# Optimization experiments

Hardware: AMD Instinct MI355X
Metric: run time of the kernel (lower is better)

Reference implementation:

```python
import jax, jax.numpy as jnp
import numpy as np

T = 1024          # num tokens
H = 2048          # hidden_size
NH = 16           # attention heads
NKV = 4           # kv heads (GQA)
HD = 128          # head_dim
E = 32            # num routed experts
K = 4             # top_k
I = 1024          # moe_intermediate_size
NS = 1            # num_shared_experts
EPS = 1e-6
THETA = 600000.0  # rope base
SCALE = HD ** -0.5


def rmsnorm(x, w):
    return x * jax.lax.rsqrt(jnp.mean(x * x, axis=-1, keepdims=True) + EPS) * w


def rope(x, positions):
    # x: [T, n_heads, HD], neox-style rotation on full head_dim
    half = HD // 2
    inv_freq = 1.0 / (THETA ** (jnp.arange(half, dtype=jnp.float32) / half))
    ang = positions.astype(jnp.float32)[:, None] * inv_freq        # [T, half]
    cos = jnp.cos(ang)[:, None, :]
    sin = jnp.sin(ang)[:, None, :]
    x1, x2 = x[..., :half], x[..., half:]
    return jnp.concatenate([x1 * cos - x2 * sin, x1 * sin + x2 * cos], axis=-1)


def setup_inputs() -> dict:
    key = jax.random.key(0)
    ks = jax.random.split(key, 10)
    s = 0.02
    return {
        "hidden_states": jax.random.normal(ks[0], (T, H), dtype=jnp.float32),
        "positions": jnp.arange(T, dtype=jnp.int32),
        "w_rms1": jnp.ones((H,), jnp.float32),
        "w_rms2": jnp.ones((H,), jnp.float32),
        "w_qkv": jax.random.normal(ks[1], ((NH + 2 * NKV) * HD, H), jnp.float32) * s,
        "w_o": jax.random.normal(ks[2], (H, NH * HD), jnp.float32) * s,
        "w_router": jax.random.normal(ks[3], (E, H), jnp.float32) * s,
        "w1": jax.random.normal(ks[4], (E, H, I), jnp.float32) * s,   # expert gate proj
        "w3": jax.random.normal(ks[5], (E, H, I), jnp.float32) * s,   # expert up proj
        "w2": jax.random.normal(ks[6], (E, I, H), jnp.float32) * s,   # expert down proj
        "ws_gate_up": jax.random.normal(ks[7], (2 * I * NS, H), jnp.float32) * s,
        "ws_down": jax.random.normal(ks[8], (H, I * NS), jnp.float32) * s,
    }


def reference(hidden_states, positions, w_rms1, w_rms2, w_qkv, w_o, w_router,
              w1, w3, w2, ws_gate_up, ws_down):
    x = hidden_states
    # ---- attention block ----
    h = rmsnorm(x, w_rms1)
    qkv = h @ w_qkv.T                                   # [T, (NH+2NKV)*HD]
    q = qkv[:, : NH * HD].reshape(T, NH, HD)
    k = qkv[:, NH * HD : (NH + NKV) * HD].reshape(T, NKV, HD)
    v = qkv[:, (NH + NKV) * HD :].reshape(T, NKV, HD)
    q = rope(q, positions)
    k = rope(k, positions)
    rep = NH // NKV
    k = jnp.repeat(k, rep, axis=1)                      # [T, NH, HD]
    v = jnp.repeat(v, rep, axis=1)
    scores = jnp.einsum("thd,shd->hts", q, k) * SCALE   # [NH, T, T]
    causal = jnp.tril(jnp.ones((T, T), dtype=bool))
    scores = jnp.where(causal, scores, -jnp.inf)
    attn = jax.nn.softmax(scores, axis=-1)
    o = jnp.einsum("hts,shd->thd", attn, v).reshape(T, NH * HD)
    x = x + o @ w_o.T                                   # residual
    # ---- MoE block ----
    h2 = rmsnorm(x, w_rms2)
    # router in fp32 (router_dtype default)
    logits = h2.astype(jnp.float32) @ w_router.T        # [T, E]
    probs = jax.nn.softmax(logits, axis=-1)
    topv, topi = jax.lax.top_k(probs, K)                # [T, K]
    topv = topv / jnp.sum(topv, axis=-1, keepdims=True)  # norm_topk_prob
    combine = jnp.zeros((T, E), jnp.float32).at[jnp.arange(T)[:, None], topi].add(topv)
    combine = combine.astype(h2.dtype)                  # routed_scaling_factor = 1.0
    g = jnp.einsum("th,ehi->tei", h2, w1)               # [T, E, I]
    u = jnp.einsum("th,ehi->tei", h2, w3)
    a = jax.nn.silu(g) * u                              # SiluAndMul
    d = jnp.einsum("tei,eih->teh", a, w2)               # [T, E, H]
    routed = jnp.einsum("teh,te->th", d, combine)
    # shared expert MLP
    gu = h2 @ ws_gate_up.T                              # [T, 2*I*NS]
    gs, us = gu[:, : I * NS], gu[:, I * NS :]
    shared = (jax.nn.silu(gs) * us) @ ws_down.T
    return x + routed + shared
```

## Files before the change

kernel.cpp:

```cpp
#include <hip/hip_runtime.h>
#include <hip/hip_bf16.h>
#include <math.h>
#include <stdint.h>

#define T_ 1024
#define H_ 2048
#define NH_ 16
#define NKV_ 4
#define HD_ 128
#define E_ 32
#define TOPK_ 4
#define I_ 1024
#define QKVN_ 3072
#define EPS_ 1e-6f
#define THETA_ 600000.0f
#define SCALE_ 0.08838834764831845f

typedef unsigned short u16;
typedef u16 u16x4 __attribute__((ext_vector_type(4)));
typedef u16 u16x8 __attribute__((ext_vector_type(8)));
typedef __bf16 bf16x8 __attribute__((ext_vector_type(8)));
typedef float f32x4 __attribute__((ext_vector_type(4)));

__device__ __forceinline__ u16 f2b(float f) {
  unsigned u = __builtin_bit_cast(unsigned, f);
  u += 0x7FFFu + ((u >> 16) & 1u);
  return (u16)(u >> 16);
}
__device__ __forceinline__ float b2f(u16 x) {
  unsigned u = ((unsigned)x) << 16;
  return __builtin_bit_cast(float, u);
}
__device__ __forceinline__ int swz8(int r) { return ((r ^ (r >> 3)) & 7) << 3; }
__device__ __forceinline__ int s2(int i) { return (i ^ (i >> 2)) & 3; }

__device__ __forceinline__ void gload16(const void* g, void* l) {
  __builtin_amdgcn_global_load_lds(
      reinterpret_cast<const __attribute__((address_space(1))) unsigned int*>(
          reinterpret_cast<uintptr_t>(g)),
      reinterpret_cast<__attribute__((address_space(3))) unsigned int*>(
          reinterpret_cast<uintptr_t>(l)),
      16, 0, 0);
}

template<int EPI, bool GATHER>
__global__ __launch_bounds__(512, 8) void moe_gemm_k(
    const u16* __restrict__ A, const float* __restrict__ B, const float* __restrict__ B2,
    float* __restrict__ O1, float* __restrict__ O2,
    int NW, int lda, int ldb, int kchunk,
    const int* __restrict__ eoff, const int* __restrict__ slots,
    const float* __restrict__ slotw, long long sBz)
{
  __shared__ u16 As[2][64 * 32];
  __shared__ u16 Bs[2][128 * 32];

  const int e = blockIdx.y >> 3;
  const int mb = blockIdx.y & 7;
  const int goff = eoff[e];
  const int Mloc = eoff[e + 1] - goff;
  const int m0 = mb * 64;
  if (m0 >= Mloc) return;

  const int xx = blockIdx.x;
  const float* Bp;
  float* Op;
  int n0;
  if constexpr (EPI == 0) {
    int wsel = xx >> 3;
    n0 = (xx & 7) * 128;
    Bp = (wsel ? B2 : B) + (long long)e * sBz;
    Op = wsel ? O2 : O1;
  } else {
    n0 = xx * 128;
    Bp = B + (long long)e * sBz;
    Op = O1;
  }
  const int k0base = blockIdx.z * kchunk;
  const u16* Ae = GATHER ? A : (A + (long long)goff * lda);

  const int tid = threadIdx.x;
  const int lane = tid & 63;
  const int wv = tid >> 6;
  const int wm = wv >> 2, wn = wv & 3;

  const u16* Abase = nullptr;
  if (wv < 4) {
    int r = wv * 16 + (lane >> 2);
    int rr = m0 + r;
    if (rr > Mloc - 1) rr = Mloc - 1;
    long long grow = GATHER ? (long long)slots[goff + rr] : (long long)rr;
    Abase = Ae + grow * (long long)lda + (((lane & 3) ^ s2(r)) << 3);
  }

  const int bn = tid & 127;
  const int bkc = tid >> 7;
  const float* Bbase = Bp + (long long)(bkc << 3) * ldb + n0 + bn;
  const int bws = bn * 32 + ((bkc ^ s2(bn)) << 3);

  float br[8];
  auto loadB = [&](int k0) {
    const float* p = Bbase + (long long)k0 * ldb;
    #pragma unroll
    for (int j = 0; j < 8; ++j) br[j] = p[(long long)j * ldb];
  };
  auto writeB = [&](int bf) {
    u16x8 o;
    #pragma unroll
    for (int j = 0; j < 8; ++j) o[j] = f2b(br[j]);
    *(u16x8*)(&Bs[bf][bws]) = o;
  };
  auto stageA = [&](int bf, int k0) {
    if (wv < 4) gload16(Abase + k0, &As[bf][wv * 512]);
  };

  f32x4 acc[2][2];
  #pragma unroll
  for (int m = 0; m < 2; ++m)
    #pragma unroll
    for (int n = 0; n < 2; ++n)
      acc[m][n] = f32x4{0.f, 0.f, 0.f, 0.f};

  const int kg = lane >> 4;
  const int cr = lane & 15;

  int aoff[2], boff[2];
  #pragma unroll
  for (int m = 0; m < 2; ++m) {
    int r = wm * 32 + m * 16 + cr;
    aoff[m] = r * 32 + ((kg ^ s2(r)) << 3);
  }
  #pragma unroll
  for (int n = 0; n < 2; ++n) {
    int c = wn * 32 + n * 16 + cr;
    boff[n] = c * 32 + ((kg ^ s2(c)) << 3);
  }

  loadB(k0base);
  stageA(0, k0base);
  writeB(0);
  __syncthreads();

  int buf = 0;
  for (int ks = 0; ks < kchunk; ks += 32) {
    bool more = (ks + 32) < kchunk;
    if (more) { loadB(k0base + ks + 32); stageA(buf ^ 1, k0base + ks + 32); }
    const u16* Ap = &As[buf][0];
    const u16* Bq = &Bs[buf][0];
    bf16x8 af[2], bfr[2];
    #pragma unroll
    for (int m = 0; m < 2; ++m)
      af[m] = __builtin_bit_cast(bf16x8, *(const u16x8*)(Ap + aoff[m]));
    #pragma unroll
    for (int n = 0; n < 2; ++n)
      bfr[n] = __builtin_bit_cast(bf16x8, *(const u16x8*)(Bq + boff[n]));
    #pragma unroll
    for (int m = 0; m < 2; ++m)
      #pragma unroll
      for (int n = 0; n < 2; ++n)
        acc[m][n] = __builtin_amdgcn_mfma_f32_16x16x32_bf16(af[m], bfr[n], acc[m][n], 0, 0, 0);
    if (more) writeB(buf ^ 1);
    __syncthreads();
    buf ^= 1;
  }

  const int rq = lane >> 4;
  #pragma unroll
  for (int m = 0; m < 2; ++m) {
    #pragma unroll
    for (int j = 0; j < 4; ++j) {
      int row = m0 + wm * 32 + m * 16 + rq * 4 + j;
      if (row >= Mloc) continue;
      if constexpr (EPI == 0) {
        float* dst = Op + (long long)(goff + row) * NW;
        #pragma unroll
        for (int n = 0; n < 2; ++n) {
          int col = n0 + wn * 32 + n * 16 + cr;
          dst[col] = acc[m][n][j];
        }
      } else {
        int tok = slots[goff + row];
        float wgt = slotw[goff + row];
        float* dst = Op + (long long)tok * NW;
        #pragma unroll
        for (int n = 0; n < 2; ++n) {
          int col = n0 + wn * 32 + n * 16 + cr;
          atomicAdd(dst + col, wgt * acc[m][n][j]);
        }
      }
    }
  }
}

template<typename TB, bool BTL, bool GROUPED, bool GATHER, int EPI>
__global__ __launch_bounds__(256) void gemm_k(
    const u16* __restrict__ A, const TB* __restrict__ B, const TB* __restrict__ B2,
    u16* __restrict__ Cb, u16* __restrict__ Cb2, float* __restrict__ Cf,
    const float* __restrict__ res1, const float* __restrict__ res2,
    int M, int N, int K, int lda, int ldb, int ldc,
    float alpha, int causal, int mbmax, int yhalf,
    const int* __restrict__ eoff, const int* __restrict__ slots,
    const float* __restrict__ slotw,
    long long sAz, long long sBz, long long sCz, int bdivz)
{
  __shared__ u16 As[2][8192];
  __shared__ u16 Bs[2][8192];

  int m0, n0, Mloc, goff = 0;
  const u16* Ae = A;
  const TB* Be = B;
  u16* Cw = Cb;
  if (GROUPED) {
    int e = blockIdx.x / mbmax;
    int mb = blockIdx.x - e * mbmax;
    goff = eoff[e];
    Mloc = eoff[e + 1] - goff;
    m0 = mb * 128;
    if (m0 >= Mloc) return;
    int by = blockIdx.y;
    if (yhalf && by >= yhalf) {
      n0 = (by - yhalf) * 128;
      Be = B2 + (long long)e * sBz;
      Cw = Cb2;
    } else {
      n0 = by * 128;
      Be = B + (long long)e * sBz;
    }
    if (!GATHER) Ae = A + (long long)goff * lda;
  } else {
    m0 = blockIdx.x * 128;
    n0 = blockIdx.y * 128;
    Mloc = M;
    long long z = blockIdx.z;
    Ae = A + z * sAz;
    Be = B + (long long)(z / bdivz) * sBz;
    if (Cb) Cw = Cb + z * sCz;
    if (causal == 1 && n0 > m0 + 127) return;
  }

  const int tid = threadIdx.x;
  const int lane = tid & 63;
  const int wv = tid >> 6;
  const int wr = wv >> 1, wc = wv & 1;

  int kend = K;
  if (causal == 2) { int ke = m0 + 128; if (ke < kend) kend = ke; }

  f32x4 acc[4][4];
  #pragma unroll
  for (int i = 0; i < 4; ++i)
    #pragma unroll
    for (int j = 0; j < 4; ++j)
      acc[i][j] = f32x4{0.f, 0.f, 0.f, 0.f};

  auto stageA = [&](int bf, int k0) {
    #pragma unroll
    for (int it = 0; it < 4; ++it) {
      int r = it * 32 + (tid >> 3);
      int kk = (tid & 7) * 8;
      int rr = m0 + r;
      if (rr > Mloc - 1) rr = Mloc - 1;
      long long row = GATHER ? (long long)slots[goff + rr] : (long long)rr;
      const u16* src = Ae + row * (long long)lda + k0 + (kk ^ swz8(r));
      gload16(src, &As[bf][it * 2048 + (tid & ~63) * 8]);
    }
  };

  float4 bregT[8];
  float brKN[32];
  u16x8 bvKN[4];

  auto loadB = [&](int bf, int k0) {
    if constexpr (BTL) {
      if constexpr (sizeof(TB) == 4) {
        const float* Bf = (const float*)Be;
        #pragma unroll
        for (int it = 0; it < 8; ++it) {
          int idx = it * 1024 + tid * 4;
          int n = idx >> 6, kk = idx & 63;
          bregT[it] = *(const float4*)(Bf + (long long)(n0 + n) * ldb + k0 + kk);
        }
      } else {
        const u16* Bb = (const u16*)Be;
        #pragma unroll
        for (int it = 0; it < 4; ++it) {
          int r = it * 32 + (tid >> 3);
          int kk = (tid & 7) * 8;
          const u16* src = Bb + (long long)(n0 + r) * ldb + k0 + (kk ^ swz8(r));
          gload16(src, &Bs[bf][it * 2048 + (tid & ~63) * 8]);
        }
      }
    } else {
      if constexpr (sizeof(TB) == 4) {
        const float* Bf = (const float*)Be;
        int n = (tid & 63) + ((tid >> 7) << 6);
        int ks = ((tid >> 6) & 1) * 32;
        const float* bp = Bf + (long long)(k0 + ks) * ldb + n0 + n;
        #pragma unroll
        for (int j = 0; j < 32; ++j) brKN[j] = bp[(long long)j * ldb];
      } else {
        const u16* Bb = (const u16*)Be;
        int nb = (tid & 15) * 8;
        int ks = (tid >> 4) * 4;
        #pragma unroll
        for (int i = 0; i < 4; ++i)
          bvKN[i] = *(const u16x8*)(Bb + (long long)(k0 + ks + i) * ldb + n0 + nb);
      }
    }
  };

  auto writeB = [&](int bf) {
    if constexpr (BTL) {
      if constexpr (sizeof(TB) == 4) {
        #pragma unroll
        for (int it = 0; it < 8; ++it) {
          int idx = it * 1024 + tid * 4;
          int n = idx >> 6, kk = idx & 63;
          float4 f = bregT[it];
          u16x4 o = u16x4{f2b(f.x), f2b(f.y), f2b(f.z), f2b(f.w)};
          *(u16x4*)(&Bs[bf][n * 64 + (kk ^ swz8(n))]) = o;
        }
      }
    } else {
      if constexpr (sizeof(TB) == 4) {
        int n = (tid & 63) + ((tid >> 7) << 6);
        int ks = ((tid >> 6) & 1) * 32;
        #pragma unroll
        for (int p = 0; p < 4; ++p) {
          u16x8 o;
          #pragma unroll
          for (int q = 0; q < 8; ++q) o[q] = f2b(brKN[p * 8 + q]);
          *(u16x8*)(&Bs[bf][n * 64 + ((ks + p * 8) ^ swz8(n))]) = o;
        }
      } else {
        int nb = (tid & 15) * 8;
        int ks = (tid >> 4) * 4;
        #pragma unroll
        for (int q = 0; q < 8; ++q) {
          int n = nb + q;
          u16x4 o = u16x4{bvKN[0][q], bvKN[1][q], bvKN[2][q], bvKN[3][q]};
          *(u16x4*)(&Bs[bf][n * 64 + (ks ^ swz8(n))]) = o;
        }
      }
    }
  };

  const int ar = (wr << 6) + (lane & 15);
  const int bc = (wc << 6) + (lane & 15);
  int aoff[4], asw[4], boff[4], bsw[4];
  #pragma unroll
  for (int m = 0; m < 4; ++m) {
    int r = ar + m * 16; aoff[m] = r * 64; asw[m] = swz8(r);
    int rb = bc + m * 16; boff[m] = rb * 64; bsw[m] = swz8(rb);
  }

  stageA(0, 0);
  loadB(0, 0);
  writeB(0);
  __syncthreads();

  int buf = 0;
  for (int k0 = 0; k0 < kend; k0 += 64) {
    int nk = k0 + 64;
    bool more = nk < kend;
    if (more) { stageA(buf ^ 1, nk); loadB(buf ^ 1, nk); }
    const u16* Ap = &As[buf][0];
    const u16* Bp = &Bs[buf][0];
    #pragma unroll
    for (int kk = 0; kk < 64; kk += 32) {
      int kb = kk + ((lane >> 4) << 3);
      bf16x8 af[4], bfr[4];
      #pragma unroll
      for (int m = 0; m < 4; ++m)
        af[m] = __builtin_bit_cast(bf16x8, *(const u16x8*)(Ap + aoff[m] + (kb ^ asw[m])));
      #pragma unroll
      for (int n = 0; n < 4; ++n)
        bfr[n] = __builtin_bit_cast(bf16x8, *(const u16x8*)(Bp + boff[n] + (kb ^ bsw[n])));
      #pragma unroll
      for (int m = 0; m < 4; ++m)
        #pragma unroll
        for (int n = 0; n < 4; ++n)
          acc[m][n] = __builtin_amdgcn_mfma_f32_16x16x32_bf16(af[m], bfr[n], acc[m][n], 0, 0, 0);
    }
    if (more) writeB(buf ^ 1);
    __syncthreads();
    buf ^= 1;
  }

  const int cr = lane & 15, rq = lane >> 4;
  #pragma unroll
  for (int m = 0; m < 4; ++m) {
    #pragma unroll
    for (int j = 0; j < 4; ++j) {
      int row = m0 + (wr << 6) + m * 16 + rq * 4 + j;
      if (row >= Mloc) continue;
      #pragma unroll
      for (int n = 0; n < 4; ++n) {
        int col = n0 + (wc << 6) + n * 16 + cr;
        float v = acc[m][n][j];
        long long o = (long long)(goff + row) * ldc + col;
        if constexpr (EPI == 0) {
          Cw[o] = f2b(v);
        } else if constexpr (EPI == 1) {
          Cw[o] = f2b(v * alpha);
        } else if constexpr (EPI == 2) {
          Cf[o] = res1[o] + v;
        } else if constexpr (EPI == 3) {
          int tok = slots[goff + row];
          float wgt = slotw[goff + row];
          atomicAdd(&Cf[(long long)tok * ldc + col], wgt * v);
        } else {
          Cf[o] = res1[o] + res2[o] + v;
        }
      }
    }
  }
}

__global__ __launch_bounds__(256) void rmsnorm_k(const float* __restrict__ x,
                                                 const float* __restrict__ w,
                                                 u16* __restrict__ outb,
                                                 float* __restrict__ outf) {
  int t = blockIdx.x;
  int tid = threadIdx.x;
  const float* xr = x + (long long)t * H_;
  float4 a = *(const float4*)(xr + tid * 8);
  float4 b = *(const float4*)(xr + tid * 8 + 4);
  float ss = a.x * a.x + a.y * a.y + a.z * a.z + a.w * a.w +
             b.x * b.x + b.y * b.y + b.z * b.z + b.w * b.w;
  #pragma unroll
  for (int o = 32; o; o >>= 1) ss += __shfl_down(ss, o);
  __shared__ float red[4];
  if ((tid & 63) == 0) red[tid >> 6] = ss;
  __syncthreads();
  float sc = rsqrtf((red[0] + red[1] + red[2] + red[3]) * (1.0f / H_) + EPS_);
  float vo[8] = {a.x, a.y, a.z, a.w, b.x, b.y, b.z, b.w};
  const float* wr = w + tid * 8;
  u16x8 ob;
  #pragma unroll
  for (int q = 0; q < 8; ++q) {
    float val = vo[q] * sc * wr[q];
    ob[q] = f2b(val);
    if (outf) outf[(long long)t * H_ + tid * 8 + q] = val;
  }
  *(u16x8*)(outb + (long long)t * H_ + tid * 8) = ob;
}

__global__ __launch_bounds__(256) void rope_k(const u16* __restrict__ qkv,
                                              const int* __restrict__ pos,
                                              u16* __restrict__ q_r,
                                              u16* __restrict__ k_r,
                                              u16* __restrict__ v_r) {
  int t = blockIdx.x;
  int tid = threadIdx.x;
  float p = (float)pos[t];
  const u16* row = qkv + (long long)t * QKVN_;
  const float cfac = logf(THETA_) * (1.0f / 64.0f);
  #pragma unroll
  for (int it = 0; it < 4; ++it) {
    int item = it * 256 + tid;
    int h = item >> 6, d = item & 63;
    float inv = expf(-cfac * (float)d);
    float ang = p * inv;
    float c = cosf(ang), s = sinf(ang);
    float x1v = b2f(row[h * 128 + d]);
    float x2v = b2f(row[h * 128 + 64 + d]);
    u16* dst = q_r + ((long long)h * T_ + t) * HD_;
    dst[d] = f2b(x1v * c - x2v * s);
    dst[d + 64] = f2b(x1v * s + x2v * c);
  }
  {
    int item = tid;
    int kv = item >> 6, d = item & 63;
    float inv = expf(-cfac * (float)d);
    float ang = p * inv;
    float c = cosf(ang), s = sinf(ang);
    float x1v = b2f(row[NH_ * HD_ + kv * 128 + d]);
    float x2v = b2f(row[NH_ * HD_ + kv * 128 + 64 + d]);
    u16* dst = k_r + ((long long)kv * T_ + t) * HD_;
    dst[d] = f2b(x1v * c - x2v * s);
    dst[d + 64] = f2b(x1v * s + x2v * c);
  }
  #pragma unroll
  for (int it = 0; it < 2; ++it) {
    int item = it * 256 + tid;
    int kv = item >> 7, d = item & 127;
    v_r[((long long)kv * T_ + t) * HD_ + d] = row[(NH_ + NKV_) * HD_ + kv * 128 + d];
  }
}

__global__ __launch_bounds__(64) void softmax_k(u16* __restrict__ P) {
  int r = blockIdx.x;
  int h = r >> 10, i = r & 1023;
  u16* row = P + ((long long)h * T_ + i) * T_;
  int lane = threadIdx.x;
  int n = i + 1;
  float vals[16];
  float mx = -1e30f;
  #pragma unroll
  for (int it = 0; it < 16; ++it) {
    int j = it * 64 + lane;
    float s = (j < n) ? b2f(row[j]) : -1e30f;
    vals[it] = s;
    mx = fmaxf(mx, s);
  }
  #pragma unroll
  for (int o = 32; o; o >>= 1) mx = fmaxf(mx, __shfl_xor(mx, o));
  float sum = 0.f;
  #pragma unroll
  for (int it = 0; it < 16; ++it) {
    int j = it * 64 + lane;
    float e = (j < n) ? __expf(vals[it] - mx) : 0.f;
    vals[it] = e;
    sum += e;
  }
  #pragma unroll
  for (int o = 32; o; o >>= 1) sum += __shfl_xor(sum, o);
  float inv = 1.f / sum;
  #pragma unroll
  for (int it = 0; it < 16; ++it) {
    int j = it * 64 + lane;
    row[j] = f2b(vals[it] * inv);
  }
}

__global__ __launch_bounds__(64) void router_k(const float* __restrict__ h2,
                                               const float* __restrict__ wr,
                                               float* __restrict__ logits) {
  int b = blockIdx.x;
  int t = b >> 5, e = b & 31;
  const float* xr = h2 + (long long)t * H_;
  const float* wv = wr + (long long)e * H_;
  int lane = threadIdx.x;
  float s = 0.f;
  #pragma unroll
  for (int it = 0; it < 8; ++it) {
    int h = it * 256 + lane * 4;
    float4 a = *(const float4*)(xr + h);
    float4 w4 = *(const float4*)(wv + h);
    s += a.x * w4.x + a.y * w4.y + a.z * w4.z + a.w * w4.w;
  }
  #pragma unroll
  for (int o = 32; o; o >>= 1) s += __shfl_xor(s, o);
  if (lane == 0) logits[b] = s;
}

__global__ __launch_bounds__(256) void topk_k(const float* __restrict__ logits,
                                              int* __restrict__ topi,
                                              float* __restrict__ topw) {
  int t = blockIdx.x * 256 + threadIdx.x;
  if (t >= T_) return;
  float l[E_];
  #pragma unroll
  for (int e = 0; e < E_; ++e) l[e] = logits[t * E_ + e];
  int sel[TOPK_];
  float sv[TOPK_];
  unsigned used = 0;
  for (int j = 0; j < TOPK_; ++j) {
    float best = -1e30f;
    int bi = 0;
    for (int e = 0; e < E_; ++e) {
      if (used & (1u << e)) continue;
      if (l[e] > best) { best = l[e]; bi = e; }
    }
    used |= 1u << bi;
    sel[j] = bi;
    sv[j] = best;
  }
  float mx = sv[0];
  float s = 0.f;
  #pragma unroll
  for (int j = 0; j < TOPK_; ++j) { sv[j] = __expf(sv[j] - mx); s += sv[j]; }
  float inv = 1.f / s;
  #pragma unroll
  for (int j = 0; j < TOPK_; ++j) {
    topi[t * TOPK_ + j] = sel[j];
    topw[t * TOPK_ + j] = sv[j] * inv;
  }
}

__global__ __launch_bounds__(256) void hist_k(const int* __restrict__ topi, int* __restrict__ cnt) {
  int idx = blockIdx.x * 256 + threadIdx.x;
  if (idx < T_ * TOPK_) atomicAdd(&cnt[topi[idx]], 1);
}

__global__ __launch_bounds__(64) void scan_k(const int* __restrict__ cnt,
                                             int* __restrict__ eoff,
                                             int* __restrict__ cursor) {
  if (threadIdx.x == 0) {
    int s = 0;
    for (int e = 0; e < E_; ++e) { eoff[e] = s; cursor[e] = s; s += cnt[e]; }
    eoff[E_] = s;
  }
}

__global__ __launch_bounds__(256) void scatter_k(const int* __restrict__ topi,
                                                 const float* __restrict__ topw,
                                                 int* __restrict__ cursor,
                                                 int* __restrict__ slots,
                                                 float* __restrict__ slotw) {
  int idx = blockIdx.x * 256 + threadIdx.x;
  if (idx >= T_ * TOPK_) return;
  int e = topi[idx];
  int pos = atomicAdd(&cursor[e], 1);
  slots[pos] = idx >> 2;
  slotw[pos] = topw[idx];
}

__global__ __launch_bounds__(256) void silumul_f_k(const float* __restrict__ g,
                                                   const float* __restrict__ u,
                                                   u16* __restrict__ a) {
  long long idx = ((long long)blockIdx.x * 256 + threadIdx.x) * 8;
  float4 g0 = *(const float4*)(g + idx);
  float4 g1 = *(const float4*)(g + idx + 4);
  float4 u0 = *(const float4*)(u + idx);
  float4 u1 = *(const float4*)(u + idx + 4);
  float gv[8] = {g0.x, g0.y, g0.z, g0.w, g1.x, g1.y, g1.z, g1.w};
  float uv[8] = {u0.x, u0.y, u0.z, u0.w, u1.x, u1.y, u1.z, u1.w};
  u16x8 o;
  #pragma unroll
  for (int q = 0; q < 8; ++q) {
    float x = gv[q];
    float sl = x / (1.f + __expf(-x));
    o[q] = f2b(sl * uv[q]);
  }
  *(u16x8*)(a + idx) = o;
}

__global__ __launch_bounds__(256) void sharedact_k(const u16* __restrict__ gu,
                                                   u16* __restrict__ act) {
  long long idx = ((long long)blockIdx.x * 256 + threadIdx.x) * 8;
  long long t = idx >> 10;
  int i = (int)(idx & 1023);
  const u16* row = gu + t * (2 * I_);
  u16x8 g = *(const u16x8*)(row + i);
  u16x8 u = *(const u16x8*)(row + I_ + i);
  u16x8 o;
  #pragma unroll
  for (int q = 0; q < 8; ++q) {
    float x = b2f(g[q]);
    float y = b2f(u[q]);
    float sl = x / (1.f + __expf(-x));
    o[q] = f2b(sl * y);
  }
  *(u16x8*)(act + t * I_ + i) = o;
}

extern "C" void kernel_launch(void* const* d_in, const int* in_sizes, int n_in,
                              void* d_out, int out_size, void* d_ws, size_t ws_size,
                              hipStream_t stream) {
  const float* x        = (const float*)d_in[0];
  const int* positions  = (const int*)d_in[1];
  const float* w_rms1   = (const float*)d_in[2];
  const float* w_rms2   = (const float*)d_in[3];
  const float* w_qkv    = (const float*)d_in[4];
  const float* w_o      = (const float*)d_in[5];
  const float* w_router = (const float*)d_in[6];
  const float* w1       = (const float*)d_in[7];
  const float* w3       = (const float*)d_in[8];
  const float* w2       = (const float*)d_in[9];
  const float* ws_gu    = (const float*)d_in[10];
  const float* ws_dn    = (const float*)d_in[11];
  float* out = (float*)d_out;

  char* ws = (char*)d_ws;
  size_t off = 0;
  auto alloc = [&](size_t bytes) {
    size_t o = off;
    off = (off + bytes + 255) & ~(size_t)255;
    return (void*)(ws + o);
  };
  u16*  h1b     = (u16*)alloc((size_t)T_ * H_ * 2);
  u16*  qkvb    = (u16*)alloc((size_t)T_ * QKVN_ * 2);
  u16*  q_r     = (u16*)alloc((size_t)NH_ * T_ * HD_ * 2);
  u16*  k_r     = (u16*)alloc((size_t)NKV_ * T_ * HD_ * 2);
  u16*  v_r     = (u16*)alloc((size_t)NKV_ * T_ * HD_ * 2);
  u16*  scoresP = (u16*)alloc((size_t)NH_ * T_ * T_ * 2);
  u16*  o_attn  = (u16*)alloc((size_t)T_ * H_ * 2);
  float* x1     = (float*)alloc((size_t)T_ * H_ * 4);
  float* h2f    = (float*)alloc((size_t)T_ * H_ * 4);
  u16*  h2b     = (u16*)alloc((size_t)T_ * H_ * 2);
  u16*  gub     = (u16*)alloc((size_t)T_ * 2 * I_ * 2);
  u16*  actsh   = (u16*)alloc((size_t)T_ * I_ * 2);
  float* logits = (float*)alloc((size_t)T_ * E_ * 4);
  int*  topi    = (int*)alloc((size_t)T_ * TOPK_ * 4);
  float* topw   = (float*)alloc((size_t)T_ * TOPK_ * 4);
  int*  cnt     = (int*)alloc(E_ * 4);
  int*  eoffp   = (int*)alloc((E_ + 1) * 4);
  int*  cursor  = (int*)alloc(E_ * 4);
  int*  slots   = (int*)alloc((size_t)T_ * TOPK_ * 4);
  float* slotw  = (float*)alloc((size_t)T_ * TOPK_ * 4);
  u16*  a_g     = (u16*)alloc((size_t)T_ * TOPK_ * I_ * 2);
  float* routed = (float*)alloc((size_t)T_ * H_ * 4);

  float* g_f32 = (float*)scoresP;
  float* u_f32 = g_f32 + (size_t)T_ * TOPK_ * I_;

  hipMemsetAsync(routed, 0, (size_t)T_ * H_ * 4, stream);
  hipMemsetAsync(cnt, 0, E_ * 4, stream);

  rmsnorm_k<<<T_, 256, 0, stream>>>(x, w_rms1, h1b, nullptr);

  gemm_k<float, true, false, false, 0><<<dim3(8, 24, 1), 256, 0, stream>>>(
      h1b, w_qkv, nullptr, qkvb, nullptr, nullptr, nullptr, nullptr,
      T_, QKVN_, H_, H_, H_, QKVN_, 1.f, 0, 1, 0, nullptr, nullptr, nullptr, 0, 0, 0, 1);

  rope_k<<<T_, 256, 0, stream>>>(qkvb, positions, q_r, k_r, v_r);

  gemm_k<u16, true, false, false, 1><<<dim3(8, 8, NH_), 256, 0, stream>>>(
      q_r, k_r, nullptr, scoresP, nullptr, nullptr, nullptr, nullptr,
      T_, T_, HD_, HD_, HD_, T_, SCALE_, 1, 1, 0, nullptr, nullptr, nullptr,
      (long long)T_ * HD_, (long long)T_ * HD_, (long long)T_ * T_, NH_ / NKV_);

  softmax_k<<<NH_ * T_, 64, 0, stream>>>(scoresP);

  gemm_k<u16, false, false, false, 0><<<dim3(8, 1, NH_), 256, 0, stream>>>(
      scoresP, v_r, nullptr, o_attn, nullptr, nullptr, nullptr, nullptr,
      T_, HD_, T_, T_, HD_, H_, 1.f, 2, 1, 0, nullptr, nullptr, nullptr,
      (long long)T_ * T_, (long long)T_ * HD_, (long long)HD_, NH_ / NKV_);

  gemm_k<float, true, false, false, 2><<<dim3(8, 16, 1), 256, 0, stream>>>(
      o_attn, w_o, nullptr, nullptr, nullptr, x1, x, nullptr,
      T_, H_, H_, H_, H_, H_, 1.f, 0, 1, 0, nullptr, nullptr, nullptr, 0, 0, 0, 1);

  rmsnorm_k<<<T_, 256, 0, stream>>>(x1, w_rms2, h2b, h2f);

  router_k<<<T_ * E_, 64, 0, stream>>>(h2f, w_router, logits);
  topk_k<<<4, 256, 0, stream>>>(logits, topi, topw);
  hist_k<<<16, 256, 0, stream>>>(topi, cnt);
  scan_k<<<1, 64, 0, stream>>>(cnt, eoffp, cursor);
  scatter_k<<<16, 256, 0, stream>>>(topi, topw, cursor, slots, slotw);

  moe_gemm_k<0, true><<<dim3(16, E_ * 8, 1), 512, 0, stream>>>(
      h2b, w1, w3, g_f32, u_f32,
      I_, H_, I_, H_, eoffp, slots, nullptr, (long long)H_ * I_);
  silumul_f_k<<<(T_ * TOPK_ * I_) / (256 * 8), 256, 0, stream>>>(g_f32, u_f32, a_g);

  moe_gemm_k<1, false><<<dim3(16, E_ * 8, 1), 512, 0, stream>>>(
      a_g, w2, nullptr, routed, nullptr,
      H_, I_, H_, I_, eoffp, slots, slotw, (long long)I_ * H_);

  gemm_k<float, true, false, false, 0><<<dim3(8, 16, 1), 256, 0, stream>>>(
      h2b, ws_gu, nullptr, gub, nullptr, nullptr, nullptr, nullptr,
      T_, 2 * I_, H_, H_, H_, 2 * I_, 1.f, 0, 1, 0, nullptr, nullptr, nullptr, 0, 0, 0, 1);
  sharedact_k<<<(T_ * I_) / (256 * 8), 256, 0, stream>>>(gub, actsh);

  gemm_k<float, true, false, false, 4><<<dim3(8, 16, 1), 256, 0, stream>>>(
      actsh, ws_dn, nullptr, nullptr, nullptr, out, x1, routed,
      T_, H_, I_, I_, I_, H_, 1.f, 0, 1, 0, nullptr, nullptr, nullptr, 0, 0, 0, 1);
}
```

Baseline: 611.9 us.

## Replace dense GEMM with 64x128 tile, 512-thread kernel and pre-transposed V

The generic 128x128 gemm_k with 256 threads and a 64-wide k-step is replaced by a specialized dense_gemm_k. The new kernel uses a 64x128 tile, 512 threads (8 waves), a 32-wide k-step and a compile-time causal mode. V is transposed into a separate buffer so the PV GEMM can load B in the same transposed layout with async global-to-LDS copies, instead of doing a strided register transpose. The aim is more blocks and waves across CUs for these modest-size GEMMs. The cost is less reuse per tile, twice as many k iterations and syncs, and an extra transpose kernel.

```diff
diff --git a/kernel.cpp b/kernel.cpp
--- a/kernel.cpp
+++ b/kernel.cpp
@@ -31,7 +31,6 @@
   unsigned u = ((unsigned)x) << 16;
   return __builtin_bit_cast(float, u);
 }
-__device__ __forceinline__ int swz8(int r) { return ((r ^ (r >> 3)) & 7) << 3; }
 __device__ __forceinline__ int s2(int i) { return (i ^ (i >> 2)) & 3; }
 
 __device__ __forceinline__ void gload16(const void* g, void* l) {
@@ -191,229 +190,169 @@
   }
 }
 
-template<typename TB, bool BTL, bool GROUPED, bool GATHER, int EPI>
-__global__ __launch_bounds__(256) void gemm_k(
-    const u16* __restrict__ A, const TB* __restrict__ B, const TB* __restrict__ B2,
-    u16* __restrict__ Cb, u16* __restrict__ Cb2, float* __restrict__ Cf,
+template<typename TB, int EPI, int CAUSAL>
+__global__ __launch_bounds__(512, 8) void dense_gemm_k(
+    const u16* __restrict__ A, const TB* __restrict__ B,
+    u16* __restrict__ Cb, float* __restrict__ Cf,
     const float* __restrict__ res1, const float* __restrict__ res2,
-    int M, int N, int K, int lda, int ldb, int ldc,
-    float alpha, int causal, int mbmax, int yhalf,
-    const int* __restrict__ eoff, const int* __restrict__ slots,
-    const float* __restrict__ slotw,
+    int K, int lda, int ldb, int ldc, float alpha,
     long long sAz, long long sBz, long long sCz, int bdivz)
 {
-  __shared__ u16 As[2][8192];
-  __shared__ u16 Bs[2][8192];
-
-  int m0, n0, Mloc, goff = 0;
-  const u16* Ae = A;
-  const TB* Be = B;
-  u16* Cw = Cb;
-  if (GROUPED) {
-    int e = blockIdx.x / mbmax;
-    int mb = blockIdx.x - e * mbmax;
-    goff = eoff[e];
-    Mloc = eoff[e + 1] - goff;
-    m0 = mb * 128;
-    if (m0 >= Mloc) return;
-    int by = blockIdx.y;
-    if (yhalf && by >= yhalf) {
-      n0 = (by - yhalf) * 128;
-      Be = B2 + (long long)e * sBz;
-      Cw = Cb2;
-    } else {
-      n0 = by * 128;
-      Be = B + (long long)e * sBz;
-    }
-    if (!GATHER) Ae = A + (long long)goff * lda;
-  } else {
-    m0 = blockIdx.x * 128;
-    n0 = blockIdx.y * 128;
-    Mloc = M;
-    long long z = blockIdx.z;
-    Ae = A + z * sAz;
-    Be = B + (long long)(z / bdivz) * sBz;
-    if (Cb) Cw = Cb + z * sCz;
-    if (causal == 1 && n0 > m0 + 127) return;
-  }
+  __shared__ u16 As[2][64 * 32];
+  __shared__ u16 Bs[2][128 * 32];
+
+  const int m0 = blockIdx.y * 64;
+  const int n0 = blockIdx.x * 128;
+  if (CAUSAL == 1 && n0 > m0 + 63) return;
+  const long long z = blockIdx.z;
+  const u16* Ae = A + z * sAz;
+  const TB* Be = B + (long long)(z / bdivz) * sBz;
+  u16* Cwb = Cb ? Cb + z * sCz : nullptr;
+
+  int kend = K;
+  if (CAUSAL == 2) { int ke = m0 + 64; if (ke < kend) kend = ke; }
 
   const int tid = threadIdx.x;
   const int lane = tid & 63;
   const int wv = tid >> 6;
-  const int wr = wv >> 1, wc = wv & 1;
-
-  int kend = K;
-  if (causal == 2) { int ke = m0 + 128; if (ke < kend) kend = ke; }
-
-  f32x4 acc[4][4];
-  #pragma unroll
-  for (int i = 0; i < 4; ++i)
-    #pragma unroll
-    for (int j = 0; j < 4; ++j)
-      acc[i][j] = f32x4{0.f, 0.f, 0.f, 0.f};
-
+  const int wm = wv >> 2, wn = wv & 3;
+
+  const u16* Abase = nullptr;
+  if (wv < 4) {
+    int r = wv * 16 + (lane >> 2);
+    Abase = Ae + (long long)(m0 + r) * lda + (((lane & 3) ^ s2(r)) << 3);
+  }
   auto stageA = [&](int bf, int k0) {
-    #pragma unroll
-    for (int it = 0; it < 4; ++it) {
-      int r = it * 32 + (tid >> 3);
-      int kk = (tid & 7) * 8;
-      int rr = m0 + r;
-      if (rr > Mloc - 1) rr = Mloc - 1;
-      long long row = GATHER ? (long long)slots[goff + rr] : (long long)rr;
-      const u16* src = Ae + row * (long long)lda + k0 + (kk ^ swz8(r));
-      gload16(src, &As[bf][it * 2048 + (tid & ~63) * 8]);
+    if (wv < 4) gload16(Abase + k0, &As[bf][wv * 512]);
+  };
+
+  const u16* Bu16base = nullptr;
+  const float* Bf32base = nullptr;
+  int bws = 0;
+  if constexpr (sizeof(TB) == 2) {
+    int r = wv * 16 + (lane >> 2);
+    Bu16base = (const u16*)Be + (long long)(n0 + r) * ldb + (((lane & 3) ^ s2(r)) << 3);
+  } else {
+    int bn = tid >> 2, bkq = tid & 3;
+    Bf32base = (const float*)Be + (long long)(n0 + bn) * ldb + (bkq << 3);
+    bws = bn * 32 + ((bkq ^ s2(bn)) << 3);
+  }
+  float br[8];
+  auto loadB = [&](int k0) {
+    const float* p = Bf32base + k0;
+    float4 a = *(const float4*)p;
+    float4 b = *(const float4*)(p + 4);
+    br[0] = a.x; br[1] = a.y; br[2] = a.z; br[3] = a.w;
+    br[4] = b.x; br[5] = b.y; br[6] = b.z; br[7] = b.w;
+  };
+  auto writeB = [&](int bf) {
+    u16x8 o;
+    #pragma unroll
+    for (int j = 0; j < 8; ++j) o[j] = f2b(br[j]);
+    *(u16x8*)(&Bs[bf][bws]) = o;
+  };
+  auto stageBu = [&](int bf, int k0) {
+    gload16(Bu16base + k0, &Bs[bf][wv * 512]);
+  };
+
+  f32x4 acc[2][2];
+  #pragma unroll
+  for (int m = 0; m < 2; ++m)
+    #pragma unroll
+    for (int n = 0; n < 2; ++n)
+      acc[m][n] = f32x4{0.f, 0.f, 0.f, 0.f};
+
+  const int kg = lane >> 4;
+  const int cr = lane & 15;
+
+  int aoff[2], boff[2];
+  #pragma unroll
+  for (int m = 0; m < 2; ++m) {
+    int r = wm * 32 + m * 16 + cr;
+    aoff[m] = r * 32 + ((kg ^ s2(r)) << 3);
+  }
+  #pragma unroll
+  for (int n = 0; n < 2; ++n) {
+    int c = wn * 32 + n * 16 + cr;
+    boff[n] = c * 32 + ((kg ^ s2(c)) << 3);
+  }
+
+  if constexpr (sizeof(TB) == 4) {
+    loadB(0); stageA(0, 0); writeB(0);
+  } else {
+    stageA(0, 0); stageBu(0, 0);
+  }
+  __syncthreads();
+
+  int buf = 0;
+  for (int ks = 0; ks < kend; ks += 32) {
+    bool more = (ks + 32) < kend;
+    if (more) {
+      if constexpr (sizeof(TB) == 4) { loadB(ks + 32); stageA(buf ^ 1, ks + 32); }
+      else { stageA(buf ^ 1, ks + 32); stageBu(buf ^ 1, ks + 32); }
     }
-  };
-
-  float4 bregT[8];
-  float brKN[32];
-  u16x8 bvKN[4];
-
-  auto loadB = [&](int bf, int k0) {
-    if constexpr (BTL) {
-      if constexpr (sizeof(TB) == 4) {
-        const float* Bf = (const float*)Be;
-        #pragma unroll
-        for (int it = 0; it < 8; ++it) {
-          int idx = it * 1024 + tid * 4;
-          int n = idx >> 6, kk = idx & 63;
-          bregT[it] = *(const float4*)(Bf + (long long)(n0 + n) * ldb + k0 + kk);
-        }
-      } else {
-        const u16* Bb = (const u16*)Be;
-        #pragma unroll
-        for (int it = 0; it < 4; ++it) {
-          int r = it * 32 + (tid >> 3);
-          int kk = (tid & 7) * 8;
-          const u16* src = Bb + (long long)(n0 + r) * ldb + k0 + (kk ^ swz8(r));
-          gload16(src, &Bs[bf][it * 2048 + (tid & ~63) * 8]);
-        }
-      }
-    } else {
-      if constexpr (sizeof(TB) == 4) {
-        const float* Bf = (const float*)Be;
-        int n = (tid & 63) + ((tid >> 7) << 6);
-        int ks = ((tid >> 6) & 1) * 32;
-        const float* bp = Bf + (long long)(k0 + ks) * ldb + n0 + n;
-        #pragma unroll
-        for (int j = 0; j < 32; ++j) brKN[j] = bp[(long long)j * ldb];
-      } else {
-        const u16* Bb = (const u16*)Be;
-        int nb = (tid & 15) * 8;
-        int ks = (tid >> 4) * 4;
-        #pragma unroll
-        for (int i = 0; i < 4; ++i)
-          bvKN[i] = *(const u16x8*)(Bb + (long long)(k0 + ks + i) * ldb + n0 + nb);
-      }
-    }
-  };
-
-  auto writeB = [&](int bf) {
-    if constexpr (BTL) {
-      if constexpr (sizeof(TB) == 4) {
-        #pragma unroll
-        for (int it = 0; it < 8; ++it) {
-          int idx = it * 1024 + tid * 4;
-          int n = idx >> 6, kk = idx & 63;
-          float4 f = bregT[it];
-          u16x4 o = u16x4{f2b(f.x), f2b(f.y), f2b(f.z), f2b(f.w)};
-          *(u16x4*)(&Bs[bf][n * 64 + (kk ^ swz8(n))]) = o;
-        }
-      }
-    } else {
-      if constexpr (sizeof(TB) == 4) {
-        int n = (tid & 63) + ((tid >> 7) << 6);
-        int ks = ((tid >> 6) & 1) * 32;
-        #pragma unroll
-        for (int p = 0; p < 4; ++p) {
-          u16x8 o;
-          #pragma unroll
-          for (int q = 0; q < 8; ++q) o[q] = f2b(brKN[p * 8 + q]);
-          *(u16x8*)(&Bs[bf][n * 64 + ((ks + p * 8) ^ swz8(n))]) = o;
-        }
-      } else {
-        int nb = (tid & 15) * 8;
-        int ks = (tid >> 4) * 4;
-        #pragma unroll
-        for (int q = 0; q < 8; ++q) {
-          int n = nb + q;
-          u16x4 o = u16x4{bvKN[0][q], bvKN[1][q], bvKN[2][q], bvKN[3][q]};
-          *(u16x4*)(&Bs[bf][n * 64 + (ks ^ swz8(n))]) = o;
-        }
-      }
-    }
-  };
-
-  const int ar = (wr << 6) + (lane & 15);
-  const int bc = (wc << 6) + (lane & 15);
-  int aoff[4], asw[4], boff[4], bsw[4];
-  #pragma unroll
-  for (int m = 0; m < 4; ++m) {
-    int r = ar + m * 16; aoff[m] = r * 64; asw[m] = swz8(r);
-    int rb = bc + m * 16; boff[m] = rb * 64; bsw[m] = swz8(rb);
-  }
-
-  stageA(0, 0);
-  loadB(0, 0);
-  writeB(0);
-  __syncthreads();
-
-  int buf = 0;
-  for (int k0 = 0; k0 < kend; k0 += 64) {
-    int nk = k0 + 64;
-    bool more = nk < kend;
-    if (more) { stageA(buf ^ 1, nk); loadB(buf ^ 1, nk); }
     const u16* Ap = &As[buf][0];
-    const u16* Bp = &Bs[buf][0];
-    #pragma unroll
-    for (int kk = 0; kk < 64; kk += 32) {
-      int kb = kk + ((lane >> 4) << 3);
-      bf16x8 af[4], bfr[4];
+    const u16* Bq = &Bs[buf][0];
+    bf16x8 af[2], bfr[2];
+    #pragma unroll
+    for (int m = 0; m < 2; ++m)
+      af[m] = __builtin_bit_cast(bf16x8, *(const u16x8*)(Ap + aoff[m]));
+    #pragma unroll
+    for (int n = 0; n < 2; ++n)
+      bfr[n] = __builtin_bit_cast(bf16x8, *(const u16x8*)(Bq + boff[n]));
+    #pragma unroll
+    for (int m = 0; m < 2; ++m)
       #pragma unroll
-      for (int m = 0; m < 4; ++m)
-        af[m] = __builtin_bit_cast(bf16x8, *(const u16x8*)(Ap + aoff[m] + (kb ^ asw[m])));
-      #pragma unroll
-      for (int n = 0; n < 4; ++n)
-        bfr[n] = __builtin_bit_cast(bf16x8, *(const u16x8*)(Bp + boff[n] + (kb ^ bsw[n])));
-      #pragma unroll
-      for (int m = 0; m < 4; ++m)
-        #pragma unroll
-        for (int n = 0; n < 4; ++n)
-          acc[m][n] = __builtin_amdgcn_mfma_f32_16x16x32_bf16(af[m], bfr[n], acc[m][n], 0, 0, 0);
-    }
-    if (more) writeB(buf ^ 1);
+      for (int n = 0; n < 2; ++n)
+        acc[m][n] = __builtin_amdgcn_mfma_f32_16x16x32_bf16(af[m], bfr[n], acc[m][n], 0, 0, 0);
+    if constexpr (sizeof(TB) == 4) { if (more) writeB(buf ^ 1); }
     __syncthreads();
     buf ^= 1;
   }
 
-  const int cr = lane & 15, rq = lane >> 4;
-  #pragma unroll
-  for (int m = 0; m < 4; ++m) {
+  const int rq = lane >> 4;
+  #pragma unroll
+  for (int m = 0; m < 2; ++m) {
     #pragma unroll
     for (int j = 0; j < 4; ++j) {
-      int row = m0 + (wr << 6) + m * 16 + rq * 4 + j;
-      if (row >= Mloc) continue;
+      int row = m0 + wm * 32 + m * 16 + rq * 4 + j;
       #pragma unroll
-      for (int n = 0; n < 4; ++n) {
-        int col = n0 + (wc << 6) + n * 16 + cr;
+      for (int n = 0; n < 2; ++n) {
+        int col = n0 + wn * 32 + n * 16 + cr;
         float v = acc[m][n][j];
-        long long o = (long long)(goff + row) * ldc + col;
+        long long o = (long long)row * ldc + col;
         if constexpr (EPI == 0) {
-          Cw[o] = f2b(v);
+          Cwb[o] = f2b(v);
         } else if constexpr (EPI == 1) {
-          Cw[o] = f2b(v * alpha);
+          Cwb[o] = f2b(v * alpha);
         } else if constexpr (EPI == 2) {
           Cf[o] = res1[o] + v;
-        } else if constexpr (EPI == 3) {
-          int tok = slots[goff + row];
-          float wgt = slotw[goff + row];
-          atomicAdd(&Cf[(long long)tok * ldc + col], wgt * v);
         } else {
           Cf[o] = res1[o] + res2[o] + v;
         }
       }
     }
   }
+}
+
+__global__ __launch_bounds__(256) void vtrans_k(const u16* __restrict__ v_r,
+                                                u16* __restrict__ v_t) {
+  __shared__ u16 t[64][72];
+  int kv = blockIdx.z;
+  int s0 = blockIdx.x * 64, d0 = blockIdx.y * 64;
+  int tid = threadIdx.x;
+  int sr = tid >> 2, dq = (tid & 3) * 16;
+  const u16* src = v_r + ((long long)kv * T_ + s0 + sr) * HD_ + d0 + dq;
+  *(u16x8*)&t[sr][dq] = *(const u16x8*)src;
+  *(u16x8*)&t[sr][dq + 8] = *(const u16x8*)(src + 8);
+  __syncthreads();
+  int dr = tid >> 2, sq = (tid & 3) * 16;
+  u16* dst = v_t + ((long long)kv * HD_ + d0 + dr) * T_ + s0 + sq;
+  u16x8 o0, o1;
+  #pragma unroll
+  for (int j = 0; j < 8; ++j) { o0[j] = t[sq + j][dr]; o1[j] = t[sq + 8 + j][dr]; }
+  *(u16x8*)dst = o0;
+  *(u16x8*)(dst + 8) = o1;
 }
 
 __global__ __launch_bounds__(256) void rmsnorm_k(const float* __restrict__ x,
@@ -674,6 +613,7 @@
   u16*  q_r     = (u16*)alloc((size_t)NH_ * T_ * HD_ * 2);
   u16*  k_r     = (u16*)alloc((size_t)NKV_ * T_ * HD_ * 2);
   u16*  v_r     = (u16*)alloc((size_t)NKV_ * T_ * HD_ * 2);
+  u16*  v_t     = (u16*)alloc((size_t)NKV_ * HD_ * T_ * 2);
   u16*  scoresP = (u16*)alloc((size_t)NH_ * T_ * T_ * 2);
   u16*  o_attn  = (u16*)alloc((size_t)T_ * H_ * 2);
   float* x1     = (float*)alloc((size_t)T_ * H_ * 4);
@@ -700,27 +640,28 @@
 
   rmsnorm_k<<<T_, 256, 0, stream>>>(x, w_rms1, h1b, nullptr);
 
-  gemm_k<float, true, false, false, 0><<<dim3(8, 24, 1), 256, 0, stream>>>(
-      h1b, w_qkv, nullptr, qkvb, nullptr, nullptr, nullptr, nullptr,
-      T_, QKVN_, H_, H_, H_, QKVN_, 1.f, 0, 1, 0, nullptr, nullptr, nullptr, 0, 0, 0, 1);
+  dense_gemm_k<float, 0, 0><<<dim3(24, 16, 1), 512, 0, stream>>>(
+      h1b, w_qkv, qkvb, nullptr, nullptr, nullptr,
+      H_, H_, H_, QKVN_, 1.f, 0, 0, 0, 1);
 
   rope_k<<<T_, 256, 0, stream>>>(qkvb, positions, q_r, k_r, v_r);
-
-  gemm_k<u16, true, false, false, 1><<<dim3(8, 8, NH_), 256, 0, stream>>>(
-      q_r, k_r, nullptr, scoresP, nullptr, nullptr, nullptr, nullptr,
-      T_, T_, HD_, HD_, HD_, T_, SCALE_, 1, 1, 0, nullptr, nullptr, nullptr,
+  vtrans_k<<<dim3(16, 2, 4), 256, 0, stream>>>(v_r, v_t);
+
+  dense_gemm_k<u16, 1, 1><<<dim3(8, 16, NH_), 512, 0, stream>>>(
+      q_r, k_r, scoresP, nullptr, nullptr, nullptr,
+      HD_, HD_, HD_, T_, SCALE_,
       (long long)T_ * HD_, (long long)T_ * HD_, (long long)T_ * T_, NH_ / NKV_);
 
   softmax_k<<<NH_ * T_, 64, 0, stream>>>(scoresP);
 
-  gemm_k<u16, false, false, false, 0><<<dim3(8, 1, NH_), 256, 0, stream>>>(
-      scoresP, v_r, nullptr, o_attn, nullptr, nullptr, nullptr, nullptr,
-      T_, HD_, T_, T_, HD_, H_, 1.f, 2, 1, 0, nullptr, nullptr, nullptr,
-      (long long)T_ * T_, (long long)T_ * HD_, (long long)HD_, NH_ / NKV_);
-
-  gemm_k<float, true, false, false, 2><<<dim3(8, 16, 1), 256, 0, stream>>>(
-      o_attn, w_o, nullptr, nullptr, nullptr, x1, x, nullptr,
-      T_, H_, H_, H_, H_, H_, 1.f, 0, 1, 0, nullptr, nullptr, nullptr, 0, 0, 0, 1);
+  dense_gemm_k<u16, 0, 2><<<dim3(1, 16, NH_), 512, 0, stream>>>(
+      scoresP, v_t, o_attn, nullptr, nullptr, nullptr,
+      T_, T_, T_, H_, 1.f,
+      (long long)T_ * T_, (long long)HD_ * T_, (long long)HD_, NH_ / NKV_);
+
+  dense_gemm_k<float, 2, 0><<<dim3(16, 16, 1), 512, 0, stream>>>(
+      o_attn, w_o, nullptr, x1, x, nullptr,
+      H_, H_, H_, H_, 1.f, 0, 0, 0, 1);
 
   rmsnorm_k<<<T_, 256, 0, stream>>>(x1, w_rms2, h2b, h2f);
 
@@ -739,12 +680,12 @@
       a_g, w2, nullptr, routed, nullptr,
       H_, I_, H_, I_, eoffp, slots, slotw, (long long)I_ * H_);
 
-  gemm_k<float, true, false, false, 0><<<dim3(8, 16, 1), 256, 0, stream>>>(
-      h2b, ws_gu, nullptr, gub, nullptr, nullptr, nullptr, nullptr,
-      T_, 2 * I_, H_, H_, H_, 2 * I_, 1.f, 0, 1, 0, nullptr, nullptr, nullptr, 0, 0, 0, 1);
+  dense_gemm_k<float, 0, 0><<<dim3(16, 16, 1), 512, 0, stream>>>(
+      h2b, ws_gu, gub, nullptr, nullptr, nullptr,
+      H_, H_, H_, 2 * I_, 1.f, 0, 0, 0, 1);
   sharedact_k<<<(T_ * I_) / (256 * 8), 256, 0, stream>>>(gub, actsh);
 
-  gemm_k<float, true, false, false, 4><<<dim3(8, 16, 1), 256, 0, stream>>>(
-      actsh, ws_dn, nullptr, nullptr, nullptr, out, x1, routed,
-      T_, H_, I_, I_, I_, H_, 1.f, 0, 1, 0, nullptr, nullptr, nullptr, 0, 0, 0, 1);
-}
+  dense_gemm_k<float, 4, 0><<<dim3(16, 16, 1), 512, 0, stream>>>(
+      actsh, ws_dn, nullptr, out, x1, routed,
+      I_, I_, I_, H_, 1.f, 0, 0, 0, 1);
+}
```

Result: no change. 616.0 us (+0.7%).
